# Performance work log

Measured on AMD Instinct MI355X. Metric: run time of the kernel, lower is better.

The kernel has to match this reference:

```python
import jax, jax.numpy as jnp
import numpy as np

B, S, HID = 2, 2048, 2048
NH, HD, G = 16, 128, 4
NKV = NH // G  # 4
ROPE_THETA = 10000.0


def _xavier(key, shape):
    fan_in, fan_out = shape
    lim = float(np.sqrt(6.0 / (fan_in + fan_out)))
    return jax.random.uniform(key, shape, jnp.float32, -lim, lim)


def setup_inputs() -> dict:
    key = jax.random.key(0)
    ks = jax.random.split(key, 6)
    hidden_states = jax.random.normal(ks[0], (B, S, HID), jnp.float32)
    # mask==True means MASKED (code adds mask * -1e9): causal upper triangle
    causal = jnp.triu(jnp.ones((S, S), jnp.bool_), k=1)
    mask = jnp.broadcast_to(causal[None, None], (B, 1, S, S))
    return {
        "hidden_states": hidden_states,
        "mask": mask,
        "Wq": _xavier(ks[1], (HID, NH * HD)),
        "bq": jnp.zeros((NH * HD,), jnp.float32),
        "Wk": _xavier(ks[2], (HID, NKV * HD)),
        "bk": jnp.zeros((NKV * HD,), jnp.float32),
        "Wv": _xavier(ks[3], (HID, NKV * HD)),
        "bv": jnp.zeros((NKV * HD,), jnp.float32),
        "Wo": _xavier(ks[4], (NH * HD, HID)),
        "bo": jnp.zeros((HID,), jnp.float32),
    }


def _rope_cos_sin(seq_len, head_dim, dtype):
    half = head_dim // 2
    inv_freq = 1.0 / (ROPE_THETA ** (jnp.arange(0, half, dtype=jnp.float32) / half))
    ang = jnp.arange(seq_len, dtype=jnp.float32)[:, None] * inv_freq[None, :]  # [S, half]
    # shape [1, S, 1, half] for broadcasting over (B, S, H, half)
    return jnp.cos(ang)[None, :, None, :].astype(dtype), jnp.sin(ang)[None, :, None, :].astype(dtype)


def _apply_rope(x, cos, sin):
    half = x.shape[-1] // 2
    x1, x2 = x[..., :half], x[..., half:]
    return jnp.concatenate([x1 * cos - x2 * sin, x1 * sin + x2 * cos], axis=-1)


def reference(hidden_states, mask, Wq, bq, Wk, bk, Wv, bv, Wo, bo):
    b, s, _ = hidden_states.shape
    scale = 1.0 / jnp.sqrt(jnp.asarray(HD, hidden_states.dtype))

    q = (hidden_states @ Wq + bq).reshape(b, s, NH, HD)
    k = (hidden_states @ Wk + bk).reshape(b, s, NKV, HD)
    v = (hidden_states @ Wv + bv).reshape(b, s, NKV, HD)

    cos, sin = _rope_cos_sin(s, HD, hidden_states.dtype)
    q = _apply_rope(q, cos, sin)
    k = _apply_rope(k, cos, sin)

    q = jnp.transpose(q, (0, 2, 1, 3))          # [B, NH, S, D]
    k = jnp.transpose(k, (0, 2, 1, 3))          # [B, NKV, S, D]
    v = jnp.transpose(v, (0, 2, 1, 3))          # [B, NKV, S, D]

    # GQA: group query heads instead of repeating K/V (same math as jnp.repeat)
    qg = q.reshape(b, NKV, G, s, HD)
    scores = jnp.einsum('bngqd,bnkd->bngqk', qg, k) * scale  # [B, NKV, G, S, S]

    maskf = mask.astype(scores.dtype)[:, :, None]  # [B, 1, 1, S, S]
    scores = scores + maskf * (-1e9)

    probs = jax.nn.softmax(scores, axis=-1)
    out = jnp.einsum('bngqk,bnkd->bngqd', probs, v)          # [B, NKV, G, S, D]
    out = out.reshape(b, NH, s, HD).transpose(0, 2, 1, 3).reshape(b, s, NH * HD)
    return out @ Wo + bo
```

## Files before the change

kernel.cpp:

```cpp
#include <hip/hip_runtime.h>
#include <hip/hip_bf16.h>

#define B_ 2
#define S_ 2048
#define HID_ 2048
#define NH_ 16
#define HD_ 128
#define NKV_ 4
#define M_ (B_*S_)
#define NQKV_ 3072
#define QSCALE2 0.12752464484148957f
#define DEFER_THR 11.5425f
#define NSPLIT 4

typedef __bf16 bf16x8 __attribute__((ext_vector_type(8)));
typedef float f32x4 __attribute__((ext_vector_type(4)));
typedef float f32x16 __attribute__((ext_vector_type(16)));

typedef __attribute__((address_space(1))) const unsigned int gas_uint;
typedef __attribute__((address_space(3))) unsigned int las_uint;

__device__ __forceinline__ unsigned short f2bfu(float x) {
  __hip_bfloat16 h = __float2bfloat16(x);
  return __builtin_bit_cast(unsigned short, h);
}

__device__ __forceinline__ unsigned int pack2bf(float lo, float hi) {
  return (unsigned int)f2bfu(lo) | ((unsigned int)f2bfu(hi) << 16);
}

__device__ __forceinline__ float bflo(unsigned int u) {
  return __builtin_bit_cast(float, u << 16);
}
__device__ __forceinline__ float bfhi(unsigned int u) {
  return __builtin_bit_cast(float, u & 0xffff0000u);
}
__device__ __forceinline__ float bf2f(unsigned short u) {
  return __builtin_bit_cast(float, (unsigned int)u << 16);
}

__device__ __forceinline__ void gload_lds16(const void* g, void* l) {
  __builtin_amdgcn_global_load_lds((gas_uint*)g, (las_uint*)l, 16, 0, 0);
}

__global__ void k_prep(const float* __restrict__ X, unsigned short* __restrict__ Xb,
                       const float* __restrict__ bq, const float* __restrict__ bk,
                       const float* __restrict__ bv, float* __restrict__ Bqkv,
                       float* __restrict__ cosT, float* __restrict__ sinT,
                       const float* __restrict__ Wq, const float* __restrict__ Wk,
                       const float* __restrict__ Wv, const float* __restrict__ Wo,
                       unsigned short* __restrict__ Wt, unsigned short* __restrict__ Wot) {
  __shared__ float t[32][33];
  int blk = blockIdx.x;
  if (blk < 8192) {
    int i = blk * 256 + threadIdx.x;
    float4 v = ((const float4*)X)[i];
    ushort4 o;
    o.x = f2bfu(v.x); o.y = f2bfu(v.y); o.z = f2bfu(v.z); o.w = f2bfu(v.w);
    ((ushort4*)Xb)[i] = o;
  } else if (blk < 8204) {
    int i = (blk - 8192) * 256 + threadIdx.x;
    float v = (i < 2048) ? bq[i] : (i < 2560 ? bk[i - 2048] : bv[i - 2560]);
    Bqkv[i] = v;
  } else if (blk < 8716) {
    int idx = (blk - 8204) * 256 + threadIdx.x;
    int s = idx >> 6, i = idx & 63;
    float invf = expf(-(float)i * (9.210340371976184f / 64.f));
    float ang = (float)s * invf;
    cosT[idx] = cosf(ang);
    sinT[idx] = sinf(ang);
  } else {
    int tb = blk - 8716;
    const float* src;
    unsigned short* dst;
    int R, C, bx, by;
    if (tb < 4096)      { src = Wq; dst = Wt;              R = 2048; C = 2048; bx = tb & 63;          by = tb >> 6; }
    else if (tb < 5120) { src = Wk; dst = Wt + 2048*2048;  R = 2048; C = 512;  int i = tb - 4096; bx = i & 15; by = i >> 4; }
    else if (tb < 6144) { src = Wv; dst = Wt + 2560*2048;  R = 2048; C = 512;  int i = tb - 5120; bx = i & 15; by = i >> 4; }
    else                { src = Wo; dst = Wot;             R = 2048; C = 2048; int i = tb - 6144; bx = i & 63; by = i >> 6; }
    int bc = bx * 32, br = by * 32;
    int tx = threadIdx.x & 31, ty = threadIdx.x >> 5;
    for (int i = ty; i < 32; i += 8)
      t[i][tx] = src[(size_t)(br + i) * C + bc + tx];
    __syncthreads();
    for (int i = ty; i < 32; i += 8)
      dst[(size_t)(bc + i) * R + br + tx] = f2bfu(t[tx][i]);
  }
}


template <int MODE>
__global__ __launch_bounds__(256, 2)
void k_gemm(const unsigned short* __restrict__ A, const unsigned short* __restrict__ Bt,
            const float* __restrict__ bias, void* __restrict__ Cv,
            int Md, int Nd, int Kd,
            const float* __restrict__ cosT, const float* __restrict__ sinT,
            unsigned short* __restrict__ Qr, unsigned short* __restrict__ Kr,
            unsigned short* __restrict__ Vt) {
  __shared__ __align__(16) unsigned short As[128 * 64];
  __shared__ __align__(16) unsigned short Bs[128 * 64];
  int nt = Nd >> 7;
  int nwg = (Md >> 7) * nt;
  int bid = blockIdx.x;
  int wg = bid;
  if ((nwg & 7) == 0) { int cpx = nwg >> 3; wg = (bid & 7) * cpx + (bid >> 3); }
  int bm = wg / nt, bn = wg - bm * nt;
  int tid = threadIdx.x;
  int lane = tid & 63, w = tid >> 6;
  int lr = lane & 15, lg = lane >> 4;
  f32x4 acc[2][8] = {};

  const int chunkbase = w << 2;
  const int boff = lane << 4;
  const int nK = Kd >> 6;
  const size_t rowstride = (size_t)Kd * 2;

  for (int kt = 0; kt < nK; ++kt) {
#pragma unroll
    for (int i = 0; i < 4; ++i) {
      int off = ((chunkbase + i) << 10) + boff;
      int row = off >> 7;
      int colb = off & 127;
      int scolb = colb ^ ((row & 7) << 4);
      const char* ga = (const char*)A + (size_t)(bm * 128 + row) * rowstride + (kt << 7) + scolb;
      const char* gb = (const char*)Bt + (size_t)(bn * 128 + row) * rowstride + (kt << 7) + scolb;
      gload_lds16(ga, (char*)As + ((chunkbase + i) << 10));
      gload_lds16(gb, (char*)Bs + ((chunkbase + i) << 10));
    }
    __syncthreads();
#pragma unroll
    for (int kk = 0; kk < 2; ++kk) {
      bf16x8 a[2], b[8];
      int kb = ((kk << 5) + (lg << 3)) << 1;
#pragma unroll
      for (int mi = 0; mi < 2; ++mi) {
        int row = (w << 5) + (mi << 4) + lr;
        a[mi] = *(const bf16x8*)((const char*)As + (row << 7) + (kb ^ ((row & 7) << 4)));
      }
#pragma unroll
      for (int ni = 0; ni < 8; ++ni) {
        int row = (ni << 4) + lr;
        b[ni] = *(const bf16x8*)((const char*)Bs + (row << 7) + (kb ^ ((row & 7) << 4)));
      }
#pragma unroll
      for (int mi = 0; mi < 2; ++mi)
#pragma unroll
        for (int ni = 0; ni < 8; ++ni)
          acc[mi][ni] = __builtin_amdgcn_mfma_f32_16x16x32_bf16(a[mi], b[ni], acc[mi][ni], 0, 0, 0);
    }
    __syncthreads();
  }

  if (MODE == 0) {
#pragma unroll
    for (int mi = 0; mi < 2; ++mi) {
      int r0 = bm * 128 + (w << 5) + (mi << 4) + (lg << 2);
#pragma unroll
      for (int ni = 0; ni < 8; ++ni) {
        int col = bn * 128 + (ni << 4) + lr;
        float bz = bias[col];
#pragma unroll
        for (int r = 0; r < 4; ++r)
          ((float*)Cv)[(size_t)(r0 + r) * Nd + col] = acc[mi][ni][r] + bz;
      }
    }
  } else if (bn >= 20) {
#pragma unroll
    for (int mi = 0; mi < 2; ++mi) {
      int r0 = bm * 128 + (w << 5) + (mi << 4) + (lg << 2);
      int s0 = r0 & (S_ - 1), bb = r0 >> 11;
#pragma unroll
      for (int ni = 0; ni < 8; ++ni) {
        int col = bn * 128 + (ni << 4) + lr;
        int cv = col - 2560;
        int kv = cv >> 7, d = cv & 127;
        float bz = bias[col];
        ushort4 o;
        o.x = f2bfu(acc[mi][ni][0] + bz);
        o.y = f2bfu(acc[mi][ni][1] + bz);
        o.z = f2bfu(acc[mi][ni][2] + bz);
        o.w = f2bfu(acc[mi][ni][3] + bz);
        *(ushort4*)(Vt + (((size_t)(bb * NKV_ + kv) * HD_ + d) << 11) + s0) = o;
      }
    }
  } else {
    bool isQ = (bn < 16);
    int hh = isQ ? bn : bn - 16;
#pragma unroll
    for (int mi = 0; mi < 2; ++mi) {
#pragma unroll
      for (int r = 0; r < 4; ++r) {
        int m = bm * 128 + (w << 5) + (mi << 4) + (lg << 2) + r;
        int s = m & (S_ - 1), bb = m >> 11;
        size_t base = isQ ? ((size_t)(bb * NH_ + hh) * S_ + s) * HD_
                          : ((size_t)(bb * NKV_ + hh) * S_ + s) * HD_;
#pragma unroll
        for (int ni = 0; ni < 4; ++ni) {
          int c = (ni << 4) + lr;
          float v1 = acc[mi][ni][r]     + bias[bn * 128 + c];
          float v2 = acc[mi][ni + 4][r] + bias[bn * 128 + c + 64];
          float cs = cosT[(s << 6) + c], sn = sinT[(s << 6) + c];
          float o1 = v1 * cs - v2 * sn;
          float o2 = v1 * sn + v2 * cs;
          if (isQ) {
            Qr[base + c]      = f2bfu(o1 * QSCALE2);
            Qr[base + c + 64] = f2bfu(o2 * QSCALE2);
          } else {
            Kr[base + c]      = f2bfu(o1);
            Kr[base + c + 64] = f2bfu(o2);
          }
        }
      }
    }
  }
}


__global__ __launch_bounds__(256, 2)
void k_attn(const unsigned short* __restrict__ Qr, const unsigned short* __restrict__ Kr,
            const unsigned short* __restrict__ Vt,
            unsigned short* __restrict__ Po0, unsigned short* __restrict__ Po1,
            unsigned short* __restrict__ Po2, unsigned short* __restrict__ Po3,
            float2* __restrict__ Ml) {
  __shared__ __align__(16) unsigned short Ks[2][64 * 128];
  int bid = blockIdx.x;
  int g = bid & 7;
  int b = g >> 2, kvh = g & 3;
  int r = bid >> 3;
  int split = r & 3;
  int r2 = r >> 2;
  int hg = r2 >> 4;
  int qt = 15 - (r2 & 15);
  int h = (kvh << 2) + hg;
  int tid = threadIdx.x, lane = tid & 63, w = tid >> 6;
  int ql = lane & 31, hi = lane >> 5;
  int q0 = (qt << 7) + (w << 5);
  int qrow = q0 + ql;

  const unsigned short* Qp = Qr + (((size_t)(b * NH_ + h) * S_) << 7);
  const unsigned short* Kp = Kr + (((size_t)(b * NKV_ + kvh) * S_) << 7);
  const unsigned short* Vp = Vt + (((size_t)(b * NKV_ + kvh) * HD_) << 11);

  bf16x8 qa[8];
#pragma unroll
  for (int c = 0; c < 8; ++c)
    qa[c] = *(const bf16x8*)(Qp + (((size_t)qrow) << 7) + (c << 4) + (hi << 3));

  f32x16 acc[4] = {};
  float m_r = -1e30f, l_r = 0.f;

  const int T = (qt + 1) << 1;
  const int nit = (T - split + 3) >> 2;

#define STAGE_K(bsel, t)                                                        \
  {                                                                             \
    const char* kbase = (const char*)Kp + ((size_t)(t) << 14);                  \
    _Pragma("unroll")                                                           \
    for (int i_ = 0; i_ < 4; ++i_) {                                            \
      int woff_ = (i_ << 12) + (w << 10);                                       \
      int off_ = woff_ + (lane << 4);                                           \
      int row_ = off_ >> 8;                                                     \
      int colb_ = off_ & 255;                                                   \
      int scolb_ = colb_ ^ ((row_ & 15) << 4);                                  \
      gload_lds16(kbase + ((size_t)row_ << 8) + scolb_,                         \
                  (char*)Ks[bsel] + woff_);                                     \
    }                                                                           \
  }

  STAGE_K(0, split);
  __syncthreads();

  for (int i = 0; i < nit; ++i) {
    int t = split + (i << 2);
    if (i + 1 < nit) STAGE_K((i + 1) & 1, t + 4);
    const char* Kb = (const char*)Ks[i & 1];

#pragma unroll
    for (int sub = 0; sub < 2; ++sub) {
      int kvbase = (t << 6) + (sub << 5);
      if (kvbase > q0 + 31) continue;

      f32x16 st = {};
      int krow = (sub << 5) + ql;
      int sw = (krow & 15) << 4;
      __builtin_amdgcn_s_setprio(1);
#pragma unroll
      for (int c = 0; c < 8; ++c) {
        int cb = (c << 5) + (hi << 4);
        bf16x8 kf = *(const bf16x8*)(Kb + (krow << 8) + (cb ^ sw));
        st = __builtin_amdgcn_mfma_f32_32x32x16_bf16(kf, qa[c], st, 0, 0, 0);
      }
      __builtin_amdgcn_s_setprio(0);
      bf16x8 vf[8];
#pragma unroll
      for (int dc = 0; dc < 4; ++dc) {
        const unsigned short* vrow = Vp + (((size_t)((dc << 5) + ql)) << 11) + kvbase + (hi << 3);
        vf[2 * dc]     = *(const bf16x8*)(vrow);
        vf[2 * dc + 1] = *(const bf16x8*)(vrow + 16);
      }
      if (kvbase + 31 > q0) {
#pragma unroll
        for (int rr = 0; rr < 16; ++rr) {
          int kv = kvbase + (rr & 3) + ((rr >> 2) << 3) + (hi << 2);
          if (kv > qrow) st[rr] = -1e30f;
        }
      }
      float pmax = st[0];
#pragma unroll
      for (int rr = 1; rr < 16; ++rr) pmax = fmaxf(pmax, st[rr]);
      pmax = fmaxf(pmax, __shfl_xor(pmax, 32));
      if (!__all(pmax <= m_r + DEFER_THR)) {
        float mn = fmaxf(m_r, pmax);
        float al = exp2f(m_r - mn);
        m_r = mn;
        l_r *= al;
#pragma unroll
        for (int dc = 0; dc < 4; ++dc) acc[dc] = acc[dc] * al;
      }
      float p[16];
      float ps = 0.f;
#pragma unroll
      for (int rr = 0; rr < 16; ++rr) { p[rr] = exp2f(st[rr] - m_r); ps += p[rr]; }
      l_r += ps;
      unsigned int W[8];
#pragma unroll
      for (int i2 = 0; i2 < 8; ++i2) W[i2] = pack2bf(p[2 * i2], p[2 * i2 + 1]);
      unsigned int e0 = __shfl_xor(hi ? W[0] : W[2], 32);
      unsigned int e1 = __shfl_xor(hi ? W[1] : W[3], 32);
      unsigned int e2 = __shfl_xor(hi ? W[4] : W[6], 32);
      unsigned int e3 = __shfl_xor(hi ? W[5] : W[7], 32);
      uint4 u0, u1;
      u0.x = hi ? e0 : W[0];
      u0.y = hi ? e1 : W[1];
      u0.z = hi ? W[2] : e0;
      u0.w = hi ? W[3] : e1;
      u1.x = hi ? e2 : W[4];
      u1.y = hi ? e3 : W[5];
      u1.z = hi ? W[6] : e2;
      u1.w = hi ? W[7] : e3;
      bf16x8 pa0 = __builtin_bit_cast(bf16x8, u0);
      bf16x8 pa1 = __builtin_bit_cast(bf16x8, u1);
      __builtin_amdgcn_s_setprio(1);
#pragma unroll
      for (int dc = 0; dc < 4; ++dc) {
        acc[dc] = __builtin_amdgcn_mfma_f32_32x32x16_bf16(vf[2 * dc], pa0, acc[dc], 0, 0, 0);
        acc[dc] = __builtin_amdgcn_mfma_f32_32x32x16_bf16(vf[2 * dc + 1], pa1, acc[dc], 0, 0, 0);
      }
      __builtin_amdgcn_s_setprio(0);
    }
    __syncthreads();
  }

  float l_tot = l_r + __shfl_xor(l_r, 32);
  unsigned short* Pob = (split == 0) ? Po0 : (split == 1) ? Po1 : (split == 2) ? Po2 : Po3;
  float inv = (l_tot > 0.f) ? (1.f / l_tot) : 0.f;
  unsigned short* obase = Pob + ((((size_t)(b * S_) + qrow)) << 11) + (h << 7) + (hi << 2);
#pragma unroll
  for (int dc = 0; dc < 4; ++dc)
#pragma unroll
    for (int gq = 0; gq < 4; ++gq) {
      ushort4 o;
      o.x = f2bfu(acc[dc][4 * gq + 0] * inv);
      o.y = f2bfu(acc[dc][4 * gq + 1] * inv);
      o.z = f2bfu(acc[dc][4 * gq + 2] * inv);
      o.w = f2bfu(acc[dc][4 * gq + 3] * inv);
      *(ushort4*)(obase + (dc << 5) + (gq << 3)) = o;
    }
  if (hi == 0)
    Ml[(size_t)split * (M_ * NH_) + ((size_t)(b * S_) + qrow) * NH_ + h] = make_float2(m_r, l_tot);
}

__global__ void k_comb(const unsigned short* __restrict__ Po0, const unsigned short* __restrict__ Po1,
                       const unsigned short* __restrict__ Po2, const unsigned short* __restrict__ Po3,
                       const float2* __restrict__ Ml, unsigned short* __restrict__ Ob) {
  int idx = blockIdx.x * 256 + threadIdx.x;
  int c = idx >> 4;
  float2 a0 = Ml[c], a1 = Ml[c + M_ * NH_], a2 = Ml[c + 2 * M_ * NH_], a3 = Ml[c + 3 * M_ * NH_];
  float m = fmaxf(fmaxf(a0.x, a1.x), fmaxf(a2.x, a3.x));
  float w0 = a0.y * exp2f(a0.x - m);
  float w1 = a1.y * exp2f(a1.x - m);
  float w2 = a2.y * exp2f(a2.x - m);
  float w3 = a3.y * exp2f(a3.x - m);
  float inv = 1.f / (w0 + w1 + w2 + w3);
  w0 *= inv; w1 *= inv; w2 *= inv; w3 *= inv;
  size_t e = (size_t)idx << 3;
  uint4 v0 = *(const uint4*)(Po0 + e);
  uint4 v1 = *(const uint4*)(Po1 + e);
  uint4 v2 = *(const uint4*)(Po2 + e);
  uint4 v3 = *(const uint4*)(Po3 + e);
  uint4 o;
  o.x = pack2bf(w0 * bflo(v0.x) + w1 * bflo(v1.x) + w2 * bflo(v2.x) + w3 * bflo(v3.x),
                w0 * bfhi(v0.x) + w1 * bfhi(v1.x) + w2 * bfhi(v2.x) + w3 * bfhi(v3.x));
  o.y = pack2bf(w0 * bflo(v0.y) + w1 * bflo(v1.y) + w2 * bflo(v2.y) + w3 * bflo(v3.y),
                w0 * bfhi(v0.y) + w1 * bfhi(v1.y) + w2 * bfhi(v2.y) + w3 * bfhi(v3.y));
  o.z = pack2bf(w0 * bflo(v0.z) + w1 * bflo(v1.z) + w2 * bflo(v2.z) + w3 * bflo(v3.z),
                w0 * bfhi(v0.z) + w1 * bfhi(v1.z) + w2 * bfhi(v2.z) + w3 * bfhi(v3.z));
  o.w = pack2bf(w0 * bflo(v0.w) + w1 * bflo(v1.w) + w2 * bflo(v2.w) + w3 * bflo(v3.w),
                w0 * bfhi(v0.w) + w1 * bfhi(v1.w) + w2 * bfhi(v2.w) + w3 * bfhi(v3.w));
  *(uint4*)(Ob + e) = o;
}


extern "C" void kernel_launch(void* const* d_in, const int* in_sizes, int n_in,
                              void* d_out, int out_size, void* d_ws, size_t ws_size,
                              hipStream_t stream) {
  const float* X  = (const float*)d_in[0];
  const float* Wq = (const float*)d_in[2];
  const float* bq = (const float*)d_in[3];
  const float* Wk = (const float*)d_in[4];
  const float* bk = (const float*)d_in[5];
  const float* Wv = (const float*)d_in[6];
  const float* bv = (const float*)d_in[7];
  const float* Wo = (const float*)d_in[8];
  const float* bo = (const float*)d_in[9];
  float* out = (float*)d_out;

  char* ws = (char*)d_ws;
  unsigned short* Xb  = (unsigned short*)(ws);
  unsigned short* Wt  = (unsigned short*)(ws + 16777216);
  unsigned short* Wot = (unsigned short*)(ws + 29360128);
  float* Bqkv         = (float*)(ws + 37748736);
  float* cosT         = (float*)(ws + 37761024);
  float* sinT         = (float*)(ws + 38285312);
  unsigned short* Qr  = (unsigned short*)(ws + 89141248);
  unsigned short* Kr  = (unsigned short*)(ws + 105918464);
  unsigned short* Vtb = (unsigned short*)(ws + 110112768);
  unsigned short* Ob  = (unsigned short*)(ws + 114307072);
  unsigned short* Po0 = (unsigned short*)(ws);
  unsigned short* Po1 = (unsigned short*)(ws + 38809600);
  unsigned short* Po2 = (unsigned short*)(ws + 38809600 + 16777216);
  unsigned short* Po3 = (unsigned short*)(ws + 38809600 + 33554432);
  float2* Ml          = (float2*)(ws + 16777216);

  k_prep<<<18956, 256, 0, stream>>>(X, Xb, bq, bk, bv, Bqkv, cosT, sinT,
                                    Wq, Wk, Wv, Wo, Wt, Wot);

  k_gemm<1><<<(M_ / 128) * (NQKV_ / 128), 256, 0, stream>>>(
      Xb, Wt, Bqkv, nullptr, M_, NQKV_, HID_, cosT, sinT, Qr, Kr, Vtb);

  k_attn<<<B_ * NH_ * (S_ / 128) * NSPLIT, 256, 0, stream>>>(Qr, Kr, Vtb, Po0, Po1, Po2, Po3, Ml);
  k_comb<<<M_ * HID_ / 8 / 256, 256, 0, stream>>>(Po0, Po1, Po2, Po3, Ml, Ob);

  k_gemm<0><<<(M_ / 128) * (HID_ / 128), 256, 0, stream>>>(
      Ob, Wot, bo, out, M_, HID_, NH_ * HD_, nullptr, nullptr, nullptr, nullptr, nullptr);
}
```

Before: 226.9 us.

## Process two 32-key subtiles jointly per softmax step in attention loop

Restructures the attention inner loop so both 32-row key subtiles of a 64-key tile are scored together. Their QK MFMAs are interleaved, one shared max and rescale pass covers both, and the PV MFMAs are issued back to back. This halves the online-softmax rescale checks and cross-lane reductions and gives more independent MFMA work to hide latency. In exchange it raises register pressure by holding two score tiles and two V fragment sets, which may reduce occupancy.

```diff
diff --git a/kernel.cpp b/kernel.cpp
--- a/kernel.cpp
+++ b/kernel.cpp
@@ -275,76 +275,139 @@
     if (i + 1 < nit) STAGE_K((i + 1) & 1, t + 4);
     const char* Kb = (const char*)Ks[i & 1];
 
-#pragma unroll
-    for (int sub = 0; sub < 2; ++sub) {
-      int kvbase = (t << 6) + (sub << 5);
-      if (kvbase > q0 + 31) continue;
-
-      f32x16 st = {};
-      int krow = (sub << 5) + ql;
-      int sw = (krow & 15) << 4;
+    int kv0 = t << 6;
+    int kv1 = kv0 + 32;
+    if (kv0 > q0 + 31) { __syncthreads(); continue; }
+    bool do1 = (kv1 <= q0 + 31);
+
+    bf16x8 vf0[8];
+#pragma unroll
+    for (int dc = 0; dc < 4; ++dc) {
+      const unsigned short* vrow = Vp + (((size_t)((dc << 5) + ql)) << 11) + kv0 + (hi << 3);
+      vf0[2 * dc]     = *(const bf16x8*)(vrow);
+      vf0[2 * dc + 1] = *(const bf16x8*)(vrow + 16);
+    }
+
+    f32x16 st0 = {}, st1 = {};
+    int krow0 = ql, krow1 = 32 + ql;
+    int sw0 = (krow0 & 15) << 4, sw1 = (krow1 & 15) << 4;
+    __builtin_amdgcn_s_setprio(1);
+#pragma unroll
+    for (int c = 0; c < 8; ++c) {
+      int cb = (c << 5) + (hi << 4);
+      bf16x8 kf0 = *(const bf16x8*)(Kb + (krow0 << 8) + (cb ^ sw0));
+      st0 = __builtin_amdgcn_mfma_f32_32x32x16_bf16(kf0, qa[c], st0, 0, 0, 0);
+      if (do1) {
+        bf16x8 kf1 = *(const bf16x8*)(Kb + (krow1 << 8) + (cb ^ sw1));
+        st1 = __builtin_amdgcn_mfma_f32_32x32x16_bf16(kf1, qa[c], st1, 0, 0, 0);
+      }
+    }
+    __builtin_amdgcn_s_setprio(0);
+
+    if (kv0 + 31 > q0) {
+#pragma unroll
+      for (int rr = 0; rr < 16; ++rr) {
+        int kv = kv0 + (rr & 3) + ((rr >> 2) << 3) + (hi << 2);
+        if (kv > qrow) st0[rr] = -1e30f;
+      }
+    }
+    if (do1 && kv1 + 31 > q0) {
+#pragma unroll
+      for (int rr = 0; rr < 16; ++rr) {
+        int kv = kv1 + (rr & 3) + ((rr >> 2) << 3) + (hi << 2);
+        if (kv > qrow) st1[rr] = -1e30f;
+      }
+    }
+
+    float pmax = st0[0];
+#pragma unroll
+    for (int rr = 1; rr < 16; ++rr) pmax = fmaxf(pmax, st0[rr]);
+    if (do1) {
+#pragma unroll
+      for (int rr = 0; rr < 16; ++rr) pmax = fmaxf(pmax, st1[rr]);
+    }
+    pmax = fmaxf(pmax, __shfl_xor(pmax, 32));
+    if (!__all(pmax <= m_r + DEFER_THR)) {
+      float mn = fmaxf(m_r, pmax);
+      float al = exp2f(m_r - mn);
+      m_r = mn;
+      l_r *= al;
+#pragma unroll
+      for (int dc = 0; dc < 4; ++dc) acc[dc] = acc[dc] * al;
+    }
+
+    float ps = 0.f;
+    float p[16];
+#pragma unroll
+    for (int rr = 0; rr < 16; ++rr) { p[rr] = exp2f(st0[rr] - m_r); ps += p[rr]; }
+    unsigned int W[8];
+#pragma unroll
+    for (int i2 = 0; i2 < 8; ++i2) W[i2] = pack2bf(p[2 * i2], p[2 * i2 + 1]);
+    unsigned int e0 = __shfl_xor(hi ? W[0] : W[2], 32);
+    unsigned int e1 = __shfl_xor(hi ? W[1] : W[3], 32);
+    unsigned int e2 = __shfl_xor(hi ? W[4] : W[6], 32);
+    unsigned int e3 = __shfl_xor(hi ? W[5] : W[7], 32);
+    uint4 u0, u1;
+    u0.x = hi ? e0 : W[0];
+    u0.y = hi ? e1 : W[1];
+    u0.z = hi ? W[2] : e0;
+    u0.w = hi ? W[3] : e1;
+    u1.x = hi ? e2 : W[4];
+    u1.y = hi ? e3 : W[5];
+    u1.z = hi ? W[6] : e2;
+    u1.w = hi ? W[7] : e3;
+    bf16x8 pa0 = __builtin_bit_cast(bf16x8, u0);
+    bf16x8 pa1 = __builtin_bit_cast(bf16x8, u1);
+
+    if (do1) {
+      bf16x8 vf1[8];
+#pragma unroll
+      for (int dc = 0; dc < 4; ++dc) {
+        const unsigned short* vrow = Vp + (((size_t)((dc << 5) + ql)) << 11) + kv1 + (hi << 3);
+        vf1[2 * dc]     = *(const bf16x8*)(vrow);
+        vf1[2 * dc + 1] = *(const bf16x8*)(vrow + 16);
+      }
+      float q2[16];
+#pragma unroll
+      for (int rr = 0; rr < 16; ++rr) { q2[rr] = exp2f(st1[rr] - m_r); ps += q2[rr]; }
+      unsigned int Y[8];
+#pragma unroll
+      for (int i2 = 0; i2 < 8; ++i2) Y[i2] = pack2bf(q2[2 * i2], q2[2 * i2 + 1]);
+      unsigned int f0 = __shfl_xor(hi ? Y[0] : Y[2], 32);
+      unsigned int f1 = __shfl_xor(hi ? Y[1] : Y[3], 32);
+      unsigned int f2 = __shfl_xor(hi ? Y[4] : Y[6], 32);
+      unsigned int f3 = __shfl_xor(hi ? Y[5] : Y[7], 32);
+      uint4 w0, w1;
+      w0.x = hi ? f0 : Y[0];
+      w0.y = hi ? f1 : Y[1];
+      w0.z = hi ? Y[2] : f0;
+      w0.w = hi ? Y[3] : f1;
+      w1.x = hi ? f2 : Y[4];
+      w1.y = hi ? f3 : Y[5];
+      w1.z = hi ? Y[6] : f2;
+      w1.w = hi ? Y[7] : f3;
+      bf16x8 pb0 = __builtin_bit_cast(bf16x8, w0);
+      bf16x8 pb1 = __builtin_bit_cast(bf16x8, w1);
+      l_r += ps;
       __builtin_amdgcn_s_setprio(1);
 #pragma unroll
-      for (int c = 0; c < 8; ++c) {
-        int cb = (c << 5) + (hi << 4);
-        bf16x8 kf = *(const bf16x8*)(Kb + (krow << 8) + (cb ^ sw));
-        st = __builtin_amdgcn_mfma_f32_32x32x16_bf16(kf, qa[c], st, 0, 0, 0);
+      for (int dc = 0; dc < 4; ++dc) {
+        acc[dc] = __builtin_amdgcn_mfma_f32_32x32x16_bf16(vf0[2 * dc], pa0, acc[dc], 0, 0, 0);
+        acc[dc] = __builtin_amdgcn_mfma_f32_32x32x16_bf16(vf0[2 * dc + 1], pa1, acc[dc], 0, 0, 0);
+      }
+#pragma unroll
+      for (int dc = 0; dc < 4; ++dc) {
+        acc[dc] = __builtin_amdgcn_mfma_f32_32x32x16_bf16(vf1[2 * dc], pb0, acc[dc], 0, 0, 0);
+        acc[dc] = __builtin_amdgcn_mfma_f32_32x32x16_bf16(vf1[2 * dc + 1], pb1, acc[dc], 0, 0, 0);
       }
       __builtin_amdgcn_s_setprio(0);
-      bf16x8 vf[8];
+    } else {
+      l_r += ps;
+      __builtin_amdgcn_s_setprio(1);
 #pragma unroll
       for (int dc = 0; dc < 4; ++dc) {
-        const unsigned short* vrow = Vp + (((size_t)((dc << 5) + ql)) << 11) + kvbase + (hi << 3);
-        vf[2 * dc]     = *(const bf16x8*)(vrow);
-        vf[2 * dc + 1] = *(const bf16x8*)(vrow + 16);
-      }
-      if (kvbase + 31 > q0) {
-#pragma unroll
-        for (int rr = 0; rr < 16; ++rr) {
-          int kv = kvbase + (rr & 3) + ((rr >> 2) << 3) + (hi << 2);
-          if (kv > qrow) st[rr] = -1e30f;
-        }
-      }
-      float pmax = st[0];
-#pragma unroll
-      for (int rr = 1; rr < 16; ++rr) pmax = fmaxf(pmax, st[rr]);
-      pmax = fmaxf(pmax, __shfl_xor(pmax, 32));
-      if (!__all(pmax <= m_r + DEFER_THR)) {
-        float mn = fmaxf(m_r, pmax);
-        float al = exp2f(m_r - mn);
-        m_r = mn;
-        l_r *= al;
-#pragma unroll
-        for (int dc = 0; dc < 4; ++dc) acc[dc] = acc[dc] * al;
-      }
-      float p[16];
-      float ps = 0.f;
-#pragma unroll
-      for (int rr = 0; rr < 16; ++rr) { p[rr] = exp2f(st[rr] - m_r); ps += p[rr]; }
-      l_r += ps;
-      unsigned int W[8];
-#pragma unroll
-      for (int i2 = 0; i2 < 8; ++i2) W[i2] = pack2bf(p[2 * i2], p[2 * i2 + 1]);
-      unsigned int e0 = __shfl_xor(hi ? W[0] : W[2], 32);
-      unsigned int e1 = __shfl_xor(hi ? W[1] : W[3], 32);
-      unsigned int e2 = __shfl_xor(hi ? W[4] : W[6], 32);
-      unsigned int e3 = __shfl_xor(hi ? W[5] : W[7], 32);
-      uint4 u0, u1;
-      u0.x = hi ? e0 : W[0];
-      u0.y = hi ? e1 : W[1];
-      u0.z = hi ? W[2] : e0;
-      u0.w = hi ? W[3] : e1;
-      u1.x = hi ? e2 : W[4];
-      u1.y = hi ? e3 : W[5];
-      u1.z = hi ? W[6] : e2;
-      u1.w = hi ? W[7] : e3;
-      bf16x8 pa0 = __builtin_bit_cast(bf16x8, u0);
-      bf16x8 pa1 = __builtin_bit_cast(bf16x8, u1);
-      __builtin_amdgcn_s_setprio(1);
-#pragma unroll
-      for (int dc = 0; dc < 4; ++dc) {
-        acc[dc] = __builtin_amdgcn_mfma_f32_32x32x16_bf16(vf[2 * dc], pa0, acc[dc], 0, 0, 0);
-        acc[dc] = __builtin_amdgcn_mfma_f32_32x32x16_bf16(vf[2 * dc + 1], pa1, acc[dc], 0, 0, 0);
+        acc[dc] = __builtin_amdgcn_mfma_f32_32x32x16_bf16(vf0[2 * dc], pa0, acc[dc], 0, 0, 0);
+        acc[dc] = __builtin_amdgcn_mfma_f32_32x32x16_bf16(vf0[2 * dc + 1], pa1, acc[dc], 0, 0, 0);
       }
       __builtin_amdgcn_s_setprio(0);
     }
```

Result: slower. 233.0 us (+2.7%).
